# Performance work log

Measured on AMD Instinct MI355X. Metric: run time of the kernel, lower is better.

Reference implementation:

```python
import jax, jax.numpy as jnp
import numpy as np

D_MODEL, NUM_HEADS, D_FF = 1024, 16, 4096
HEAD_DIM = D_MODEL // NUM_HEADS
EPS = 1e-5


def _layernorm(x, g, b):
    m = jnp.mean(x, axis=-1, keepdims=True)
    v = jnp.mean((x - m) ** 2, axis=-1, keepdims=True)
    return (x - m) * jax.lax.rsqrt(v + EPS) * g + b


def setup_inputs() -> dict:
    key = jax.random.key(0)
    ks = jax.random.split(key, 16)
    N, S = 4, 2048
    x = jax.random.normal(ks[0], (N, S, D_MODEL), dtype=jnp.float32)
    # mask broadcastable against energy of shape (N, S, H, H) -- see notes: code
    # computes per-position head-vs-head attention, not SxS attention.
    mask = jax.random.randint(ks[1], (N, 1, 1, NUM_HEADS), 0, 2, dtype=jnp.int32)
    s = 0.02
    return {
        "x": x,
        "Wqkv": jax.random.normal(ks[2], (D_MODEL, 3 * D_MODEL), dtype=jnp.float32) * s,
        "bqkv": jnp.zeros((3 * D_MODEL,), jnp.float32),
        "Wo": jax.random.normal(ks[3], (D_MODEL, D_MODEL), dtype=jnp.float32) * s,
        "bo": jnp.zeros((D_MODEL,), jnp.float32),
        "g1": jnp.ones((D_MODEL,), jnp.float32),
        "beta1": jnp.zeros((D_MODEL,), jnp.float32),
        "W1": jax.random.normal(ks[4], (D_MODEL, D_FF), dtype=jnp.float32) * s,
        "bf1": jnp.zeros((D_FF,), jnp.float32),
        "W2": jax.random.normal(ks[5], (D_FF, D_MODEL), dtype=jnp.float32) * s,
        "bf2": jnpp if False else jnp.zeros((D_MODEL,), jnp.float32),
        "g2": jnp.ones((D_MODEL,), jnp.float32),
        "beta2": jnp.zeros((D_MODEL,), jnp.float32),
        "mask": mask,
    }


def reference(x, Wqkv, bqkv, Wo, bo, g1, beta1, W1, bf1, W2, bf2, g2, beta2, mask):
    N, S, D = x.shape
    H, hd = NUM_HEADS, HEAD_DIM
    # fused QKV projection
    qkv = (x @ Wqkv + bqkv).reshape(N, S, 3, H, hd).transpose(2, 0, 3, 1, 4)
    q, k, v = qkv[0], qkv[1], qkv[2]  # each (N, H, S, hd)
    # faithful to torch einsum 'nqhd,nkhd->nhqk' on (N,H,S,hd) operands:
    # energy[n,s,i,j] = sum_d q[n,i,s,d] * k[n,j,s,d]  -> (N, S, H, H)
    energy = jnp.einsum('nise,njse->nsij', q, k)
    energy = jnp.where(mask == 0, jnp.float32(-1e20), energy)
    attn = jax.nn.softmax(energy / np.sqrt(hd).astype(np.float32), axis=3)
    # torch einsum 'nhql,nlhd->nqhd': out[n,i,s,d] = sum_l attn[n,s,i,l]*v[n,l,s,d]
    out = jnp.einsum('nsil,nlse->nise', attn, v)  # (N, H, S, hd)
    out = out.reshape(N, S, D)  # row-major flatten, exactly as torch .reshape
    attn_out = out @ Wo + bo
    h = _layernorm(attn_out + x, g1, beta1)
    ff = jax.nn.relu(h @ W1 + bf1) @ W2 + bf2  # dropout = identity (eval)
    return _layernorm(ff + h, g2, beta2)
```

## Files before the change

### kernel.cpp

```cpp
#include <hip/hip_runtime.h>
#include <cstdint>
#include <cstddef>


using f32x4  = __attribute__((ext_vector_type(4))) float;
using bf16x8 = __attribute__((ext_vector_type(8))) __bf16;

__device__ __forceinline__ unsigned short f2b(float f) {
  union { float f; uint32_t u; } v; v.f = f;
  uint32_t r = v.u + 0x7FFFu + ((v.u >> 16) & 1u);
  return (unsigned short)(r >> 16);
}
__device__ __forceinline__ float b2f(unsigned short u) {
  union { uint32_t u; float f; } v; v.u = ((uint32_t)u) << 16;
  return v.f;
}

__device__ __forceinline__ void gload_lds16(const unsigned short* g,
                                            unsigned short* l) {
  __builtin_amdgcn_global_load_lds(
      (const __attribute__((address_space(1))) unsigned int*)g,
      (__attribute__((address_space(3))) unsigned int*)l, 16, 0, 0);
}

__device__ __forceinline__ void barrier_sync() {
  __builtin_amdgcn_sched_barrier(0);
  __builtin_amdgcn_s_barrier();
  __builtin_amdgcn_sched_barrier(0);
}
template <int N>
__device__ __forceinline__ void vmwait() {
  __builtin_amdgcn_sched_barrier(0);
  if constexpr (N == 0) asm volatile("s_waitcnt vmcnt(0)");
  if constexpr (N == 4) asm volatile("s_waitcnt vmcnt(4)");
  __builtin_amdgcn_sched_barrier(0);
}

__global__ __launch_bounds__(256) void prep_kernel(
    const float* __restrict__ Wqkv, unsigned short* __restrict__ WqkvT,
    const float* __restrict__ Wo,   unsigned short* __restrict__ WoT,
    const float* __restrict__ W1,   unsigned short* __restrict__ W1T,
    const float* __restrict__ W2,   unsigned short* __restrict__ W2T,
    const float* __restrict__ x,    unsigned short* __restrict__ xb) {
  __shared__ float tile[32][33];
  const int b = blockIdx.x, tid = threadIdx.x;
  if (b >= 12288) {
    for (int i = (b - 12288) * 256 + tid; i < 2097152; i += 2048 * 256) {
      float4 v = ((const float4*)x)[i];
      uint32_t lo = (uint32_t)f2b(v.x) | ((uint32_t)f2b(v.y) << 16);
      uint32_t hi = (uint32_t)f2b(v.z) | ((uint32_t)f2b(v.w) << 16);
      ((uint2*)xb)[i] = make_uint2(lo, hi);
    }
    return;
  }
  const float* W; unsigned short* WT; int K, N, jb, kb;
  if (b < 3072)       { W=Wqkv; WT=WqkvT; K=1024; N=3072; jb=b%96;          kb=b/96; }
  else if (b < 4096)  { W=Wo;   WT=WoT;   K=1024; N=1024; jb=(b-3072)%32;   kb=(b-3072)/32; }
  else if (b < 8192)  { W=W1;   WT=W1T;   K=1024; N=4096; jb=(b-4096)%128;  kb=(b-4096)/128; }
  else                { W=W2;   WT=W2T;   K=4096; N=1024; jb=(b-8192)%32;   kb=(b-8192)/32; }
  const int j0 = jb * 32, k0 = kb * 32;
  const int tx = tid & 31, ty = tid >> 5;
#pragma unroll
  for (int i = 0; i < 4; ++i)
    tile[ty + 8 * i][tx] = W[(size_t)(k0 + ty + 8 * i) * N + j0 + tx];
  __syncthreads();
#pragma unroll
  for (int i = 0; i < 4; ++i)
    WT[(size_t)(j0 + ty + 8 * i) * K + k0 + tx] = f2b(tile[tx][ty + 8 * i]);
}

template <bool SPLITK, bool OUTB, bool RELU>
__global__ __launch_bounds__(512, 2) void gemm2p_kernel(
    const unsigned short* __restrict__ A, const unsigned short* __restrict__ B,
    const float* __restrict__ bias, void* __restrict__ C,
    unsigned short* __restrict__ Cp1, unsigned short* __restrict__ Cp2,
    int M, int N, int Ks, int Kd, int nbn) {
  constexpr int HT = 128 * 64;
  __shared__ unsigned short lds[8 * HT];

  const int tid  = threadIdx.x;
  const int lane = tid & 63, wave = tid >> 6;
  const int wm = wave >> 2, wn = wave & 3;
  const int lr = lane & 15, lk = lane >> 4;
  const int x7 = lr & 7;

  const int nwg = gridDim.x, cpx = nwg >> 3, id = blockIdx.x;
  const int wg = (id & 7) * cpx + (id >> 3);
  int bm, bn, sk;
  if (SPLITK) { bm = wg >> 3; bn = (wg & 7) >> 1; sk = wg & 1; }
  else        { bm = wg / nbn; bn = wg % nbn; sk = 0; }

  const unsigned short* Ab = A + (size_t)bm * 256 * Ks + (size_t)sk * Kd;
  const unsigned short* Bb = B + (size_t)bn * 256 * Ks + (size_t)sk * Kd;

  const int srow = tid >> 3;
  const int scol = ((tid & 7) ^ (srow & 7)) * 8;
  const int ldst = wave * 8 * 64;

  const int NT = Kd >> 6;

  f32x4 acc[8][4] = {};
  bf16x8 aC[4][2], bH[2][2], bC[2][2];

#define SLOT_A(B_, H_) (((B_)*4 + (H_)) * HT)
#define SLOT_B(B_, H_) (((B_)*4 + 2 + (H_)) * HT)
#define STG_A(B_, H_, T_)                                                     \
  _Pragma("unroll") for (int i_ = 0; i_ < 2; ++i_)                            \
      gload_lds16(Ab + (size_t)((H_)*128 + i_ * 64 + srow) * Ks + (T_)*64 + scol, \
                  &lds[SLOT_A(B_, H_) + i_ * 64 * 64 + ldst])
#define STG_B(B_, H_, T_)                                                     \
  _Pragma("unroll") for (int i_ = 0; i_ < 2; ++i_)                            \
      gload_lds16(Bb + (size_t)((H_)*128 + i_ * 64 + srow) * Ks + (T_)*64 + scol, \
                  &lds[SLOT_B(B_, H_) + i_ * 64 * 64 + ldst])
#define RDA_K(DST, B_, H_, KK)                                                \
  _Pragma("unroll") for (int mi_ = 0; mi_ < 4; ++mi_)                         \
      DST[mi_][KK] = *(const bf16x8*)&lds[SLOT_A(B_, H_) +                    \
          (wm * 64 + mi_ * 16 + lr) * 64 + (((KK)*4 + lk) ^ x7) * 8]
#define RDB_K(DST, B_, H_, KK)                                                \
  _Pragma("unroll") for (int ni_ = 0; ni_ < 2; ++ni_)                         \
      DST[ni_][KK] = *(const bf16x8*)&lds[SLOT_B(B_, H_) +                    \
          (wn * 32 + ni_ * 16 + lr) * 64 + (((KK)*4 + lk) ^ x7) * 8]
#define MM8(AS, BS, MH, NH, KK)                                               \
  _Pragma("unroll") for (int mi_ = 0; mi_ < 4; ++mi_)                         \
    _Pragma("unroll") for (int ni_ = 0; ni_ < 2; ++ni_)                       \
      acc[(MH)*4 + mi_][(NH)*2 + ni_] =                                       \
          __builtin_amdgcn_mfma_f32_16x16x32_bf16(                            \
              AS[mi_][KK], BS[ni_][KK], acc[(MH)*4 + mi_][(NH)*2 + ni_], 0, 0, 0)
#define SB0() __builtin_amdgcn_sched_barrier(0)

  STG_A(0, 0, 0); STG_B(0, 0, 0); STG_B(0, 1, 0); STG_A(0, 1, 0);
  STG_A(1, 0, 1); STG_B(1, 0, 1);
  vmwait<4>();
  barrier_sync();

  for (int t = 0; t < NT; ++t) {
    const int p = t & 1;
    const bool s1 = (t + 1 < NT), s2 = (t + 2 < NT);
    if (s1) { STG_A(p ^ 1, 1, t + 1); STG_B(p ^ 1, 1, t + 1); }
    RDA_K(aC, p, 0, 0); RDB_K(bH, p, 0, 0);
    RDA_K(aC, p, 0, 1); RDB_K(bH, p, 0, 1);
    RDB_K(bC, p, 1, 0); RDB_K(bC, p, 1, 1);
    barrier_sync();
    __builtin_amdgcn_s_setprio(1);
    MM8(aC, bH, 0, 0, 0); SB0();
    MM8(aC, bH, 0, 0, 1); SB0();
    MM8(aC, bC, 0, 1, 0); SB0();
    MM8(aC, bC, 0, 1, 1);
    __builtin_amdgcn_s_setprio(0);
    barrier_sync();
    if (s2) { STG_A(p, 0, t + 2); STG_B(p, 0, t + 2); }
    RDA_K(aC, p, 1, 0); RDA_K(aC, p, 1, 1);
    if (s2) vmwait<4>(); else if (s1) vmwait<0>();
    barrier_sync();
    __builtin_amdgcn_s_setprio(1);
    MM8(aC, bC, 1, 1, 0); SB0();
    MM8(aC, bH, 1, 0, 0); SB0();
    MM8(aC, bC, 1, 1, 1); SB0();
    MM8(aC, bH, 1, 0, 1);
    __builtin_amdgcn_s_setprio(0);
    barrier_sync();
  }

#undef SB0
#undef MM8
#undef RDA_K
#undef RDB_K
#undef STG_A
#undef STG_B
#undef SLOT_A
#undef SLOT_B

  const int orow0 = bm * 256 + wm * 64;
  const int ocol0 = bn * 256 + wn * 32;
#pragma unroll
  for (int mh = 0; mh < 2; ++mh)
#pragma unroll
    for (int nh = 0; nh < 2; ++nh)
#pragma unroll
      for (int ni = 0; ni < 2; ++ni) {
        int col = ocol0 + nh * 128 + ni * 16 + lr;
        float bv = bias[col];
#pragma unroll
        for (int mi = 0; mi < 4; ++mi)
#pragma unroll
          for (int r = 0; r < 4; ++r) {
            int row = orow0 + mh * 128 + mi * 16 + lk * 4 + r;
            float val = acc[mh * 4 + mi][nh * 2 + ni][r];
            if (SPLITK) {
              unsigned short* dst = sk ? Cp2 : Cp1;
              dst[(size_t)row * N + col] = f2b(sk ? val : val + bv);
            } else {
              val += bv;
              if (RELU) val = fmaxf(val, 0.f);
              if (OUTB)
                ((unsigned short*)C)[(size_t)row * N + col] = f2b(val);
              else
                ((float*)C)[(size_t)row * N + col] = val;
            }
          }
      }
}

__global__ __launch_bounds__(256) void attn_kernel(
    const unsigned short* __restrict__ qkv, const int* __restrict__ mask,
    unsigned short* __restrict__ outb) {
  __shared__ float sq[16][68], sk[16][68], sv[16][68];
  __shared__ float sp[16][17];
  const int pos = blockIdx.x;
  const int n = pos >> 11, s = pos & 2047;
  const int tid = threadIdx.x;
  const unsigned short* row = qkv + (size_t)pos * 3072;
#pragma unroll
  for (int it = 0; it < 3; ++it) {
    uint2 raw = *(const uint2*)(row + it * 1024 + tid * 4);
    float f0 = b2f((unsigned short)(raw.x & 0xffffu));
    float f1 = b2f((unsigned short)(raw.x >> 16));
    float f2 = b2f((unsigned short)(raw.y & 0xffffu));
    float f3 = b2f((unsigned short)(raw.y >> 16));
    float(*dst)[68] = (it == 0) ? sq : (it == 1) ? sk : sv;
    int r = tid >> 4, d = (tid & 15) * 4;
    dst[r][d] = f0; dst[r][d + 1] = f1; dst[r][d + 2] = f2; dst[r][d + 3] = f3;
  }
  __syncthreads();
  {
    const int i = tid >> 4, j = tid & 15;
    float e = 0.f;
#pragma unroll
    for (int d = 0; d < 64; d += 4) {
      float4 qa = *(const float4*)&sq[i][d];
      float4 kb = *(const float4*)&sk[j][d];
      e += qa.x * kb.x + qa.y * kb.y + qa.z * kb.z + qa.w * kb.w;
    }
    if (mask[n * 16 + j] == 0) e = -1e20f;
    e *= 0.125f;
    float mx = e;
#pragma unroll
    for (int o = 8; o > 0; o >>= 1) mx = fmaxf(mx, __shfl_xor(mx, o, 16));
    float pe = __expf(e - mx);
    float sm = pe;
#pragma unroll
    for (int o = 8; o > 0; o >>= 1) sm += __shfl_xor(sm, o, 16);
    sp[i][j] = pe / sm;
  }
  __syncthreads();
  {
    const int w = tid >> 6, d = tid & 63;
    float o0 = 0, o1 = 0, o2 = 0, o3 = 0;
#pragma unroll
    for (int l = 0; l < 16; ++l) {
      float vv = sv[l][d];
      o0 += sp[w][l] * vv;      o1 += sp[w + 4][l] * vv;
      o2 += sp[w + 8][l] * vv;  o3 += sp[w + 12][l] * vv;
    }
    outb[(((size_t)n * 16 + w     ) * 2048 + s) * 64 + d] = f2b(o0);
    outb[(((size_t)n * 16 + w + 4 ) * 2048 + s) * 64 + d] = f2b(o1);
    outb[(((size_t)n * 16 + w + 8 ) * 2048 + s) * 64 + d] = f2b(o2);
    outb[(((size_t)n * 16 + w + 12) * 2048 + s) * 64 + d] = f2b(o3);
  }
}

template <bool RB16>
__global__ __launch_bounds__(256) void ln_kernel(
    const unsigned short* __restrict__ P1, const unsigned short* __restrict__ P2,
    const void* __restrict__ R,
    const float* __restrict__ g, const float* __restrict__ be,
    float* __restrict__ outf, unsigned short* __restrict__ outb) {
  const int row = blockIdx.x, tid = threadIdx.x;
  const size_t base = (size_t)row * 1024 + tid * 4;
  uint2 p = *(const uint2*)(P1 + base);
  uint2 q = *(const uint2*)(P2 + base);
  float x0 = b2f((unsigned short)(p.x & 0xffffu)) + b2f((unsigned short)(q.x & 0xffffu));
  float x1 = b2f((unsigned short)(p.x >> 16))     + b2f((unsigned short)(q.x >> 16));
  float x2 = b2f((unsigned short)(p.y & 0xffffu)) + b2f((unsigned short)(q.y & 0xffffu));
  float x3 = b2f((unsigned short)(p.y >> 16))     + b2f((unsigned short)(q.y >> 16));
  if (RB16) {
    uint2 r = *(const uint2*)((const unsigned short*)R + base);
    x0 += b2f((unsigned short)(r.x & 0xffffu));
    x1 += b2f((unsigned short)(r.x >> 16));
    x2 += b2f((unsigned short)(r.y & 0xffffu));
    x3 += b2f((unsigned short)(r.y >> 16));
  } else {
    float4 r = *(const float4*)((const float*)R + base);
    x0 += r.x; x1 += r.y; x2 += r.z; x3 += r.w;
  }
  float s = x0 + x1 + x2 + x3;
#pragma unroll
  for (int o = 32; o > 0; o >>= 1) s += __shfl_xor(s, o);
  __shared__ float red[4];
  const int lane = tid & 63, wv = tid >> 6;
  if (lane == 0) red[wv] = s;
  __syncthreads();
  float mean = (red[0] + red[1] + red[2] + red[3]) * (1.f / 1024.f);
  float d0 = x0 - mean, d1 = x1 - mean, d2 = x2 - mean, d3 = x3 - mean;
  float qd = d0 * d0 + d1 * d1 + d2 * d2 + d3 * d3;
#pragma unroll
  for (int o = 32; o > 0; o >>= 1) qd += __shfl_xor(qd, o);
  __syncthreads();
  if (lane == 0) red[wv] = qd;
  __syncthreads();
  float var = (red[0] + red[1] + red[2] + red[3]) * (1.f / 1024.f);
  float rs = rsqrtf(var + 1e-5f);
  const int col = tid * 4;
  float4 gv = *(const float4*)(g + col);
  float4 bv = *(const float4*)(be + col);
  float y0 = d0 * rs * gv.x + bv.x;
  float y1 = d1 * rs * gv.y + bv.y;
  float y2 = d2 * rs * gv.z + bv.z;
  float y3 = d3 * rs * gv.w + bv.w;
  if (outf) *(float4*)(outf + base) = make_float4(y0, y1, y2, y3);
  if (outb) {
    uint32_t lo = (uint32_t)f2b(y0) | ((uint32_t)f2b(y1) << 16);
    uint32_t hi = (uint32_t)f2b(y2) | ((uint32_t)f2b(y3) << 16);
    *(uint2*)(outb + base) = make_uint2(lo, hi);
  }
}

extern "C" void kernel_launch(void* const* d_in, const int* in_sizes, int n_in,
                              void* d_out, int out_size, void* d_ws,
                              size_t ws_size, hipStream_t stream) {
  (void)in_sizes; (void)n_in; (void)out_size; (void)ws_size;
  const float* x     = (const float*)d_in[0];
  const float* Wqkv  = (const float*)d_in[1];
  const float* bqkv  = (const float*)d_in[2];
  const float* Wo    = (const float*)d_in[3];
  const float* bo    = (const float*)d_in[4];
  const float* g1    = (const float*)d_in[5];
  const float* beta1 = (const float*)d_in[6];
  const float* W1    = (const float*)d_in[7];
  const float* bf1   = (const float*)d_in[8];
  const float* W2    = (const float*)d_in[9];
  const float* bf2   = (const float*)d_in[10];
  const float* g2    = (const float*)d_in[11];
  const float* beta2 = (const float*)d_in[12];
  const int*   mask  = (const int*)d_in[13];
  float* out = (float*)d_out;

  char* ws = (char*)d_ws;
  unsigned short* WqkvT = (unsigned short*)(ws + 0);
  unsigned short* WoT   = (unsigned short*)(ws + 6291456);
  unsigned short* W1T   = (unsigned short*)(ws + 8388608);
  unsigned short* W2T   = (unsigned short*)(ws + 16777216);
  unsigned short* xb    = (unsigned short*)(ws + 25165824);
  unsigned short* h_b   = (unsigned short*)(ws + 41943040);
  unsigned short* aop1  = (unsigned short*)(ws + 58720256);
  unsigned short* aop2  = (unsigned short*)(ws + 75497472);
  unsigned short* qkvb  = (unsigned short*)(ws + 92274688);
  unsigned short* aob   = (unsigned short*)(ws + 142606336);
  unsigned short* ff1   = qkvb;
  unsigned short* ffp1  = aop1;
  unsigned short* ffp2  = aop2;

  prep_kernel<<<14336, 256, 0, stream>>>(Wqkv, WqkvT, Wo, WoT, W1, W1T, W2, W2T, x, xb);

  gemm2p_kernel<false, true, false><<<dim3(384), 512, 0, stream>>>(
      xb, WqkvT, bqkv, qkvb, nullptr, nullptr, 8192, 3072, 1024, 1024, 12);
  attn_kernel<<<8192, 256, 0, stream>>>(qkvb, mask, aob);
  gemm2p_kernel<true, false, false><<<dim3(256), 512, 0, stream>>>(
      aob, WoT, bo, nullptr, aop1, aop2, 8192, 1024, 1024, 512, 4);
  ln_kernel<false><<<8192, 256, 0, stream>>>(aop1, aop2, x, g1, beta1, nullptr, h_b);
  gemm2p_kernel<false, true, true><<<dim3(512), 512, 0, stream>>>(
      h_b, W1T, bf1, ff1, nullptr, nullptr, 8192, 4096, 1024, 1024, 16);
  gemm2p_kernel<true, false, false><<<dim3(256), 512, 0, stream>>>(
      ff1, W2T, bf2, nullptr, ffp1, ffp2, 8192, 1024, 4096, 2048, 4);
  ln_kernel<true><<<8192, 256, 0, stream>>>(ffp1, ffp2, h_b, g2, beta2, out, nullptr);
}
```

Before: 299.6 us.

## Restructure GEMM main loop into eight-phase ping-pong schedule with register prefetch

Rewrites the GEMM inner loop so that each 64-wide K tile is consumed in eight quarter-block MFMA phases separated by barriers. LDS reads for the next phase and global-to-LDS stages for future tiles are interleaved between those phases, and the first fragments of the next tile are prefetched into registers at the end of the current iteration. The intent is finer-grained overlap of LDS reads, global loads and MFMA work, with smaller per-K fragment registers. In exchange it adds more barriers per iteration and a full vmcnt(0) wait mid-loop, which may stall.

```diff
diff --git a/kernel.cpp b/kernel.cpp
--- a/kernel.cpp
+++ b/kernel.cpp
@@ -70,7 +70,7 @@
 }
 
 template <bool SPLITK, bool OUTB, bool RELU>
-__global__ __launch_bounds__(512, 2) void gemm2p_kernel(
+__global__ __launch_bounds__(512, 2) void gemmr_kernel(
     const unsigned short* __restrict__ A, const unsigned short* __restrict__ B,
     const float* __restrict__ bias, void* __restrict__ C,
     unsigned short* __restrict__ Cp1, unsigned short* __restrict__ Cp2,
@@ -100,7 +100,7 @@
   const int NT = Kd >> 6;
 
   f32x4 acc[8][4] = {};
-  bf16x8 aC[4][2], bH[2][2], bC[2][2];
+  bf16x8 aX[4], aY[4], bP[2], bQ[2], bR[2];
 
 #define SLOT_A(B_, H_) (((B_)*4 + (H_)) * HT)
 #define SLOT_B(B_, H_) (((B_)*4 + 2 + (H_)) * HT)
@@ -112,59 +112,69 @@
   _Pragma("unroll") for (int i_ = 0; i_ < 2; ++i_)                            \
       gload_lds16(Bb + (size_t)((H_)*128 + i_ * 64 + srow) * Ks + (T_)*64 + scol, \
                   &lds[SLOT_B(B_, H_) + i_ * 64 * 64 + ldst])
-#define RDA_K(DST, B_, H_, KK)                                                \
+#define RD_A(DST, B_, H_, KK)                                                 \
   _Pragma("unroll") for (int mi_ = 0; mi_ < 4; ++mi_)                         \
-      DST[mi_][KK] = *(const bf16x8*)&lds[SLOT_A(B_, H_) +                    \
+      DST[mi_] = *(const bf16x8*)&lds[SLOT_A(B_, H_) +                        \
           (wm * 64 + mi_ * 16 + lr) * 64 + (((KK)*4 + lk) ^ x7) * 8]
-#define RDB_K(DST, B_, H_, KK)                                                \
+#define RD_B(DST, B_, H_, KK)                                                 \
   _Pragma("unroll") for (int ni_ = 0; ni_ < 2; ++ni_)                         \
-      DST[ni_][KK] = *(const bf16x8*)&lds[SLOT_B(B_, H_) +                    \
+      DST[ni_] = *(const bf16x8*)&lds[SLOT_B(B_, H_) +                        \
           (wn * 32 + ni_ * 16 + lr) * 64 + (((KK)*4 + lk) ^ x7) * 8]
-#define MM8(AS, BS, MH, NH, KK)                                               \
-  _Pragma("unroll") for (int mi_ = 0; mi_ < 4; ++mi_)                         \
-    _Pragma("unroll") for (int ni_ = 0; ni_ < 2; ++ni_)                       \
-      acc[(MH)*4 + mi_][(NH)*2 + ni_] =                                       \
-          __builtin_amdgcn_mfma_f32_16x16x32_bf16(                            \
-              AS[mi_][KK], BS[ni_][KK], acc[(MH)*4 + mi_][(NH)*2 + ni_], 0, 0, 0)
-#define SB0() __builtin_amdgcn_sched_barrier(0)
-
-  STG_A(0, 0, 0); STG_B(0, 0, 0); STG_B(0, 1, 0); STG_A(0, 1, 0);
-  STG_A(1, 0, 1); STG_B(1, 0, 1);
+#define MM8(AS, BS, MH, NH)                                                   \
+  do {                                                                        \
+    __builtin_amdgcn_s_setprio(1);                                            \
+    _Pragma("unroll") for (int mi_ = 0; mi_ < 4; ++mi_)                       \
+      _Pragma("unroll") for (int ni_ = 0; ni_ < 2; ++ni_)                     \
+        acc[(MH)*4 + mi_][(NH)*2 + ni_] =                                     \
+            __builtin_amdgcn_mfma_f32_16x16x32_bf16(                          \
+                AS[mi_], BS[ni_], acc[(MH)*4 + mi_][(NH)*2 + ni_], 0, 0, 0);  \
+    __builtin_amdgcn_s_setprio(0);                                            \
+  } while (0)
+
+  STG_A(0, 0, 0); STG_B(0, 0, 0); STG_A(0, 1, 0); STG_B(0, 1, 0);
+  STG_A(1, 1, 1); STG_B(1, 1, 1);
   vmwait<4>();
   barrier_sync();
+  RD_A(aX, 0, 0, 0);
+  RD_B(bP, 0, 0, 0);
+  RD_B(bQ, 0, 1, 0);
 
   for (int t = 0; t < NT; ++t) {
     const int p = t & 1;
     const bool s1 = (t + 1 < NT), s2 = (t + 2 < NT);
-    if (s1) { STG_A(p ^ 1, 1, t + 1); STG_B(p ^ 1, 1, t + 1); }
-    RDA_K(aC, p, 0, 0); RDB_K(bH, p, 0, 0);
-    RDA_K(aC, p, 0, 1); RDB_K(bH, p, 0, 1);
-    RDB_K(bC, p, 1, 0); RDB_K(bC, p, 1, 1);
-    barrier_sync();
-    __builtin_amdgcn_s_setprio(1);
-    MM8(aC, bH, 0, 0, 0); SB0();
-    MM8(aC, bH, 0, 0, 1); SB0();
-    MM8(aC, bC, 0, 1, 0); SB0();
-    MM8(aC, bC, 0, 1, 1);
-    __builtin_amdgcn_s_setprio(0);
-    barrier_sync();
-    if (s2) { STG_A(p, 0, t + 2); STG_B(p, 0, t + 2); }
-    RDA_K(aC, p, 1, 0); RDA_K(aC, p, 1, 1);
-    if (s2) vmwait<4>(); else if (s1) vmwait<0>();
-    barrier_sync();
-    __builtin_amdgcn_s_setprio(1);
-    MM8(aC, bC, 1, 1, 0); SB0();
-    MM8(aC, bH, 1, 0, 0); SB0();
-    MM8(aC, bC, 1, 1, 1); SB0();
-    MM8(aC, bH, 1, 0, 1);
-    __builtin_amdgcn_s_setprio(0);
-    barrier_sync();
-  }
-
-#undef SB0
+    RD_A(aY, p, 1, 0);
+    if (s1) STG_A(p ^ 1, 0, t + 1);
+    barrier_sync();
+    MM8(aX, bP, 0, 0);
+    if (s1) STG_B(p ^ 1, 0, t + 1);
+    barrier_sync();
+    MM8(aX, bQ, 0, 1);
+    RD_A(aX, p, 1, 1);
+    RD_B(bR, p, 0, 1);
+    barrier_sync();
+    MM8(aY, bQ, 1, 1);
+    RD_B(bQ, p, 1, 1);
+    barrier_sync();
+    MM8(aY, bP, 1, 0);
+    RD_A(aY, p, 0, 1);
+    barrier_sync();
+    MM8(aX, bR, 1, 0);
+    vmwait<0>();
+    barrier_sync();
+    MM8(aX, bQ, 1, 1);
+    if (s1) { RD_A(aX, p ^ 1, 0, 0); RD_B(bP, p ^ 1, 0, 0); }
+    if (s2) STG_A(p, 1, t + 2);
+    barrier_sync();
+    MM8(aY, bQ, 0, 1);
+    if (s1) RD_B(bQ, p ^ 1, 1, 0);
+    if (s2) STG_B(p, 1, t + 2);
+    barrier_sync();
+    MM8(aY, bR, 0, 0);
+  }
+
 #undef MM8
-#undef RDA_K
-#undef RDB_K
+#undef RD_A
+#undef RD_B
 #undef STG_A
 #undef STG_B
 #undef SLOT_A
@@ -352,15 +362,15 @@
 
   prep_kernel<<<14336, 256, 0, stream>>>(Wqkv, WqkvT, Wo, WoT, W1, W1T, W2, W2T, x, xb);
 
-  gemm2p_kernel<false, true, false><<<dim3(384), 512, 0, stream>>>(
+  gemmr_kernel<false, true, false><<<dim3(384), 512, 0, stream>>>(
       xb, WqkvT, bqkv, qkvb, nullptr, nullptr, 8192, 3072, 1024, 1024, 12);
   attn_kernel<<<8192, 256, 0, stream>>>(qkvb, mask, aob);
-  gemm2p_kernel<true, false, false><<<dim3(256), 512, 0, stream>>>(
+  gemmr_kernel<true, false, false><<<dim3(256), 512, 0, stream>>>(
       aob, WoT, bo, nullptr, aop1, aop2, 8192, 1024, 1024, 512, 4);
   ln_kernel<false><<<8192, 256, 0, stream>>>(aop1, aop2, x, g1, beta1, nullptr, h_b);
-  gemm2p_kernel<false, true, true><<<dim3(512), 512, 0, stream>>>(
+  gemmr_kernel<false, true, true><<<dim3(512), 512, 0, stream>>>(
       h_b, W1T, bf1, ff1, nullptr, nullptr, 8192, 4096, 1024, 1024, 16);
-  gemm2p_kernel<true, false, false><<<dim3(256), 512, 0, stream>>>(
+  gemmr_kernel<true, false, false><<<dim3(256), 512, 0, stream>>>(
       ff1, W2T, bf2, nullptr, ffp1, ffp2, 8192, 1024, 4096, 2048, 4);
   ln_kernel<true><<<8192, 256, 0, stream>>>(ffp1, ffp2, h_b, g2, beta2, out, nullptr);
 }
```

After: 291.0 us. -2.9%, faster.

## Restructure GEMM main loop prefetching and split-K the QKV projection

Applied to the files above, without the earlier changes.

The GEMM main loop is rescheduled to keep two A register sets and to prefetch the next tile's LDS fragments into registers during the current tile's MFMAs. It uses finer vmcnt waits and fewer barriers per iteration. The QKV projection becomes a 2-way split-K launch with 768 workgroups writing two bf16 partials, which the attention kernel sums when loading. This aims to improve latency hiding and wave fill for the QKV GEMM. The cost is more register pressure, extra partial-sum traffic, and two rounded bf16 partials in place of one.

```diff
diff --git a/kernel.cpp b/kernel.cpp
--- a/kernel.cpp
+++ b/kernel.cpp
@@ -32,7 +32,8 @@
 __device__ __forceinline__ void vmwait() {
   __builtin_amdgcn_sched_barrier(0);
   if constexpr (N == 0) asm volatile("s_waitcnt vmcnt(0)");
-  if constexpr (N == 4) asm volatile("s_waitcnt vmcnt(4)");
+  if constexpr (N == 2) asm volatile("s_waitcnt vmcnt(2)");
+  if constexpr (N == 6) asm volatile("s_waitcnt vmcnt(6)");
   __builtin_amdgcn_sched_barrier(0);
 }
 
@@ -70,7 +71,7 @@
 }
 
 template <bool SPLITK, bool OUTB, bool RELU>
-__global__ __launch_bounds__(512, 2) void gemm2p_kernel(
+__global__ __launch_bounds__(512, 2) void gemm2s_kernel(
     const unsigned short* __restrict__ A, const unsigned short* __restrict__ B,
     const float* __restrict__ bias, void* __restrict__ C,
     unsigned short* __restrict__ Cp1, unsigned short* __restrict__ Cp2,
@@ -87,7 +88,7 @@
   const int nwg = gridDim.x, cpx = nwg >> 3, id = blockIdx.x;
   const int wg = (id & 7) * cpx + (id >> 3);
   int bm, bn, sk;
-  if (SPLITK) { bm = wg >> 3; bn = (wg & 7) >> 1; sk = wg & 1; }
+  if (SPLITK) { sk = wg & 1; bn = (wg >> 1) % nbn; bm = (wg >> 1) / nbn; }
   else        { bm = wg / nbn; bn = wg % nbn; sk = 0; }
 
   const unsigned short* Ab = A + (size_t)bm * 256 * Ks + (size_t)sk * Kd;
@@ -100,7 +101,7 @@
   const int NT = Kd >> 6;
 
   f32x4 acc[8][4] = {};
-  bf16x8 aC[4][2], bH[2][2], bC[2][2];
+  bf16x8 aA[4][2], aB[4][2], bH[2][2], bC[2][2];
 
 #define SLOT_A(B_, H_) (((B_)*4 + (H_)) * HT)
 #define SLOT_B(B_, H_) (((B_)*4 + 2 + (H_)) * HT)
@@ -112,14 +113,16 @@
   _Pragma("unroll") for (int i_ = 0; i_ < 2; ++i_)                            \
       gload_lds16(Bb + (size_t)((H_)*128 + i_ * 64 + srow) * Ks + (T_)*64 + scol, \
                   &lds[SLOT_B(B_, H_) + i_ * 64 * 64 + ldst])
-#define RDA_K(DST, B_, H_, KK)                                                \
-  _Pragma("unroll") for (int mi_ = 0; mi_ < 4; ++mi_)                         \
-      DST[mi_][KK] = *(const bf16x8*)&lds[SLOT_A(B_, H_) +                    \
-          (wm * 64 + mi_ * 16 + lr) * 64 + (((KK)*4 + lk) ^ x7) * 8]
-#define RDB_K(DST, B_, H_, KK)                                                \
-  _Pragma("unroll") for (int ni_ = 0; ni_ < 2; ++ni_)                         \
-      DST[ni_][KK] = *(const bf16x8*)&lds[SLOT_B(B_, H_) +                    \
-          (wn * 32 + ni_ * 16 + lr) * 64 + (((KK)*4 + lk) ^ x7) * 8]
+#define RD_A(DST, B_, H_)                                                     \
+  _Pragma("unroll") for (int kk_ = 0; kk_ < 2; ++kk_)                         \
+    _Pragma("unroll") for (int mi_ = 0; mi_ < 4; ++mi_)                       \
+      DST[mi_][kk_] = *(const bf16x8*)&lds[SLOT_A(B_, H_) +                   \
+          (wm * 64 + mi_ * 16 + lr) * 64 + ((kk_ * 4 + lk) ^ x7) * 8]
+#define RD_B(DST, B_, H_)                                                     \
+  _Pragma("unroll") for (int kk_ = 0; kk_ < 2; ++kk_)                         \
+    _Pragma("unroll") for (int ni_ = 0; ni_ < 2; ++ni_)                       \
+      DST[ni_][kk_] = *(const bf16x8*)&lds[SLOT_B(B_, H_) +                   \
+          (wn * 32 + ni_ * 16 + lr) * 64 + ((kk_ * 4 + lk) ^ x7) * 8]
 #define MM8(AS, BS, MH, NH, KK)                                               \
   _Pragma("unroll") for (int mi_ = 0; mi_ < 4; ++mi_)                         \
     _Pragma("unroll") for (int ni_ = 0; ni_ < 2; ++ni_)                       \
@@ -128,43 +131,45 @@
               AS[mi_][KK], BS[ni_][KK], acc[(MH)*4 + mi_][(NH)*2 + ni_], 0, 0, 0)
 #define SB0() __builtin_amdgcn_sched_barrier(0)
 
-  STG_A(0, 0, 0); STG_B(0, 0, 0); STG_B(0, 1, 0); STG_A(0, 1, 0);
-  STG_A(1, 0, 1); STG_B(1, 0, 1);
-  vmwait<4>();
+  STG_A(0, 0, 0); STG_B(0, 0, 0); STG_B(0, 1, 0);
+  STG_A(0, 1, 0);
+  vmwait<2>();
   barrier_sync();
+  RD_A(aA, 0, 0); RD_B(bH, 0, 0); RD_B(bC, 0, 1);
+  STG_A(1, 0, 1); STG_B(1, 0, 1); STG_B(1, 1, 1);
 
   for (int t = 0; t < NT; ++t) {
     const int p = t & 1;
     const bool s1 = (t + 1 < NT), s2 = (t + 2 < NT);
-    if (s1) { STG_A(p ^ 1, 1, t + 1); STG_B(p ^ 1, 1, t + 1); }
-    RDA_K(aC, p, 0, 0); RDB_K(bH, p, 0, 0);
-    RDA_K(aC, p, 0, 1); RDB_K(bH, p, 0, 1);
-    RDB_K(bC, p, 1, 0); RDB_K(bC, p, 1, 1);
+    vmwait<6>();
     barrier_sync();
+    RD_A(aB, p, 1);
+    if (s1) STG_A(p ^ 1, 1, t + 1);
+    SB0();
     __builtin_amdgcn_s_setprio(1);
-    MM8(aC, bH, 0, 0, 0); SB0();
-    MM8(aC, bH, 0, 0, 1); SB0();
-    MM8(aC, bC, 0, 1, 0); SB0();
-    MM8(aC, bC, 0, 1, 1);
+    MM8(aA, bH, 0, 0, 0); MM8(aA, bH, 0, 0, 1);
+    MM8(aA, bC, 0, 1, 0); MM8(aA, bC, 0, 1, 1);
     __builtin_amdgcn_s_setprio(0);
+    vmwait<2>();
     barrier_sync();
-    if (s2) { STG_A(p, 0, t + 2); STG_B(p, 0, t + 2); }
-    RDA_K(aC, p, 1, 0); RDA_K(aC, p, 1, 1);
-    if (s2) vmwait<4>(); else if (s1) vmwait<0>();
-    barrier_sync();
+    if (s1) RD_A(aA, p ^ 1, 0);
+    if (s2) { STG_A(p, 0, t + 2); STG_B(p, 0, t + 2); STG_B(p, 1, t + 2); }
+    SB0();
     __builtin_amdgcn_s_setprio(1);
-    MM8(aC, bC, 1, 1, 0); SB0();
-    MM8(aC, bH, 1, 0, 0); SB0();
-    MM8(aC, bC, 1, 1, 1); SB0();
-    MM8(aC, bH, 1, 0, 1);
+    MM8(aB, bC, 1, 1, 0); MM8(aB, bC, 1, 1, 1);
     __builtin_amdgcn_s_setprio(0);
-    barrier_sync();
+    if (s1) RD_B(bC, p ^ 1, 1);
+    SB0();
+    __builtin_amdgcn_s_setprio(1);
+    MM8(aB, bH, 1, 0, 0); MM8(aB, bH, 1, 0, 1);
+    __builtin_amdgcn_s_setprio(0);
+    if (s1) RD_B(bH, p ^ 1, 0);
   }
 
 #undef SB0
 #undef MM8
-#undef RDA_K
-#undef RDB_K
+#undef RD_A
+#undef RD_B
 #undef STG_A
 #undef STG_B
 #undef SLOT_A
@@ -202,21 +207,23 @@
 }
 
 __global__ __launch_bounds__(256) void attn_kernel(
-    const unsigned short* __restrict__ qkv, const int* __restrict__ mask,
-    unsigned short* __restrict__ outb) {
+    const unsigned short* __restrict__ qkv1, const unsigned short* __restrict__ qkv2,
+    const int* __restrict__ mask, unsigned short* __restrict__ outb) {
   __shared__ float sq[16][68], sk[16][68], sv[16][68];
   __shared__ float sp[16][17];
   const int pos = blockIdx.x;
   const int n = pos >> 11, s = pos & 2047;
   const int tid = threadIdx.x;
-  const unsigned short* row = qkv + (size_t)pos * 3072;
+  const unsigned short* r1 = qkv1 + (size_t)pos * 3072;
+  const unsigned short* r2 = qkv2 + (size_t)pos * 3072;
 #pragma unroll
   for (int it = 0; it < 3; ++it) {
-    uint2 raw = *(const uint2*)(row + it * 1024 + tid * 4);
-    float f0 = b2f((unsigned short)(raw.x & 0xffffu));
-    float f1 = b2f((unsigned short)(raw.x >> 16));
-    float f2 = b2f((unsigned short)(raw.y & 0xffffu));
-    float f3 = b2f((unsigned short)(raw.y >> 16));
+    uint2 a = *(const uint2*)(r1 + it * 1024 + tid * 4);
+    uint2 b = *(const uint2*)(r2 + it * 1024 + tid * 4);
+    float f0 = b2f((unsigned short)(a.x & 0xffffu)) + b2f((unsigned short)(b.x & 0xffffu));
+    float f1 = b2f((unsigned short)(a.x >> 16))     + b2f((unsigned short)(b.x >> 16));
+    float f2 = b2f((unsigned short)(a.y & 0xffffu)) + b2f((unsigned short)(b.y & 0xffffu));
+    float f3 = b2f((unsigned short)(a.y >> 16))     + b2f((unsigned short)(b.y >> 16));
     float(*dst)[68] = (it == 0) ? sq : (it == 1) ? sk : sv;
     int r = tid >> 4, d = (tid & 15) * 4;
     dst[r][d] = f0; dst[r][d + 1] = f1; dst[r][d + 2] = f2; dst[r][d + 3] = f3;
@@ -346,21 +353,22 @@
   unsigned short* aop2  = (unsigned short*)(ws + 75497472);
   unsigned short* qkvb  = (unsigned short*)(ws + 92274688);
   unsigned short* aob   = (unsigned short*)(ws + 142606336);
+  unsigned short* qkvb2 = (unsigned short*)(ws + 41943040);
   unsigned short* ff1   = qkvb;
   unsigned short* ffp1  = aop1;
   unsigned short* ffp2  = aop2;
 
   prep_kernel<<<14336, 256, 0, stream>>>(Wqkv, WqkvT, Wo, WoT, W1, W1T, W2, W2T, x, xb);
 
-  gemm2p_kernel<false, true, false><<<dim3(384), 512, 0, stream>>>(
-      xb, WqkvT, bqkv, qkvb, nullptr, nullptr, 8192, 3072, 1024, 1024, 12);
-  attn_kernel<<<8192, 256, 0, stream>>>(qkvb, mask, aob);
-  gemm2p_kernel<true, false, false><<<dim3(256), 512, 0, stream>>>(
+  gemm2s_kernel<true, false, false><<<dim3(768), 512, 0, stream>>>(
+      xb, WqkvT, bqkv, nullptr, qkvb, qkvb2, 8192, 3072, 1024, 512, 12);
+  attn_kernel<<<8192, 256, 0, stream>>>(qkvb, qkvb2, mask, aob);
+  gemm2s_kernel<true, false, false><<<dim3(256), 512, 0, stream>>>(
       aob, WoT, bo, nullptr, aop1, aop2, 8192, 1024, 1024, 512, 4);
   ln_kernel<false><<<8192, 256, 0, stream>>>(aop1, aop2, x, g1, beta1, nullptr, h_b);
-  gemm2p_kernel<false, true, true><<<dim3(512), 512, 0, stream>>>(
+  gemm2s_kernel<false, true, true><<<dim3(512), 512, 0, stream>>>(
       h_b, W1T, bf1, ff1, nullptr, nullptr, 8192, 4096, 1024, 1024, 16);
-  gemm2p_kernel<true, false, false><<<dim3(256), 512, 0, stream>>>(
+  gemm2s_kernel<true, false, false><<<dim3(256), 512, 0, stream>>>(
       ff1, W2T, bf2, nullptr, ffp1, ffp2, 8192, 1024, 4096, 2048, 4);
   ln_kernel<true><<<8192, 256, 0, stream>>>(ffp1, ffp2, h_b, g2, beta2, out, nullptr);
 }
```

Result: no change. 305.1 us (+1.8%).
